# Kernel optimization log

Measured on AMD Instinct MI355X. Metric: run time of the kernel, lower is better.

The kernel has to match this reference:

```python
import jax, jax.numpy as jnp
import numpy as np

N_NODES = 100000
N_EDGES = 1600000
IN_C, HID_C, OUT_C = 128, 128, 64


def gcn_conv(x, W, b, src, dst, n_nodes):
    """PyG-style GCNConv: h = x @ W; add self-loops; symmetric deg^-1/2 norm;
    scatter-add aggregation; + bias. Self-loop contribution added analytically
    (norm for self-loop edge i->i is deg_i^-1) instead of materializing edges."""
    h = x @ W  # [N, C_out]
    # degree over dst including self-loops (edge weights are all ones)
    deg = jax.ops.segment_sum(jnp.ones((src.shape[0],), h.dtype), dst,
                              num_segments=n_nodes) + 1.0
    dinv = jax.lax.rsqrt(deg)  # deg >= 1 always
    norm = dinv[src] * dinv[dst]  # [E]
    agg = jax.ops.segment_sum(h[src] * norm[:, None], dst, num_segments=n_nodes)
    agg = agg + h * (dinv * dinv)[:, None]  # self-loop term
    return agg + b


def setup_inputs() -> dict:
    key = jax.random.key(0)
    k0, k1, k2, k3, k4, k5 = jax.random.split(key, 6)
    x = jax.random.normal(k0, (N_NODES, IN_C), dtype=jnp.float32)
    edge_index = jax.random.randint(k1, (2, N_EDGES), 0, N_NODES, dtype=jnp.int64)
    s1 = 1.0 / np.sqrt(IN_C)
    s2 = 1.0 / np.sqrt(HID_C)
    W1 = jax.random.uniform(k2, (IN_C, HID_C), jnp.float32, -s1, s1)
    b1 = jax.random.uniform(k3, (HID_C,), jnp.float32, -s1, s1)
    W2 = jax.random.uniform(k4, (HID_C, OUT_C), jnp.float32, -s2, s2)
    b2 = jax.random.uniform(k5, (OUT_C,), jnp.float32, -s2, s2)
    return {"x": x, "W1": W1, "b1": b1, "W2": W2, "b2": b2,
            "edge_index": edge_index}


def reference(x, W1, b1, W2, b2, edge_index):
    src, dst = edge_index[0], edge_index[1]
    h = gcn_conv(x, W1, b1, src, dst, N_NODES)
    h = jax.nn.relu(h)
    out = gcn_conv(h, W2, b2, src, dst, N_NODES)
    return out
```

## Files before the change

kernel.cpp:

```cpp
#include <hip/hip_runtime.h>


static constexpr int BSHIFT = 7;
static constexpr int BWIDTH = 1 << BSHIFT;
static constexpr int MAXBUCK = 2048;
static constexpr int NPART = 256;

static constexpr size_t OFF_ROW  = 458752;
static constexpr size_t OFF_CCNT = 925696;
static constexpr size_t OFF_COFF = 937984;
static constexpr size_t OFF_DINV = 962560;
static constexpr size_t OFF_CSR  = 1376256;
static constexpr size_t OFF_HS1  = 8388608;
static constexpr size_t OFF_PART = 35651584;
static constexpr size_t OFF_HS2  = 62914560;
static constexpr size_t OFF_H2   = 75714560;
static constexpr size_t OFF_W1S  = 77811712;
static constexpr size_t OFF_W2S  = 77844480;

__device__ __forceinline__ unsigned short f2bf(float f) {
    unsigned u = __float_as_uint(f);
    u += 0x7fffu + ((u >> 16) & 1u);
    return (unsigned short)(u >> 16);
}

typedef __attribute__((ext_vector_type(8))) short bf16x8;
typedef __attribute__((ext_vector_type(4))) float f32x4;

__device__ __forceinline__ unsigned detect_flag(const unsigned* __restrict__ w) {
    unsigned fl = 0;
#pragma unroll
    for (int k = 1; k < 32; k += 2) fl |= w[k];
    return fl;
}

__device__ __forceinline__ int edge_dst(const unsigned* w, unsigned flag,
                                        int e, int E) {
    return flag ? (int)w[E + e] : (int)w[2 * E + 2 * e];
}
__device__ __forceinline__ int edge_src(const unsigned* w, unsigned flag,
                                        int e, int E) {
    return flag ? (int)w[e] : (int)w[2 * e];
}

__global__ __launch_bounds__(1024) void hist_wprep_kernel(
    const unsigned* __restrict__ w, unsigned* __restrict__ ccnt,
    unsigned* __restrict__ h2, int E, int nbuck,
    const float* __restrict__ W1, const float* __restrict__ W2,
    unsigned short* __restrict__ O1, unsigned short* __restrict__ O2) {
    if (blockIdx.x >= NPART) {
        const int which = blockIdx.x - NPART;
        const float* W = which ? W2 : W1;
        unsigned short* O = which ? O2 : O1;
        const int BN = which ? 64 : 128;
        const int total = 128 * BN / 4;
        for (int g = threadIdx.x; g < total; g += 1024) {
            int n = g % BN, k0 = (g / BN) * 4;
            ushort4 u;
            u.x = f2bf(W[(size_t)(k0 + 0) * BN + n]);
            u.y = f2bf(W[(size_t)(k0 + 1) * BN + n]);
            u.z = f2bf(W[(size_t)(k0 + 2) * BN + n]);
            u.w = f2bf(W[(size_t)(k0 + 3) * BN + n]);
            int off = ((((n >> 4) * 4 + (k0 >> 5)) * 16 + (n & 15)) * 4 +
                       ((k0 >> 3) & 3)) * 8 + (k0 & 4);
            *(ushort4*)(O + off) = u;
        }
        return;
    }
    __shared__ unsigned hist[MAXBUCK];
    for (int i = threadIdx.x; i < nbuck; i += 1024) hist[i] = 0;
    __syncthreads();
    const unsigned f = detect_flag(w);
    const int per = (E + NPART - 1) / NPART;
    const int e0 = blockIdx.x * per, e1 = min(E, e0 + per);
    for (int e = e0 + (int)threadIdx.x; e < e1; e += 1024)
        atomicAdd(&hist[edge_dst(w, f, e, E) >> BSHIFT], 1u);
    __syncthreads();
    for (int i = threadIdx.x; i < nbuck; i += 1024) {
        unsigned h = hist[i];
        h2[(size_t)i * NPART + blockIdx.x] = h;
        if (h) atomicAdd(&ccnt[i], h);
    }
}

__global__ __launch_bounds__(NPART) void scanoff_kernel(
    const unsigned* __restrict__ ccnt, unsigned* __restrict__ coff,
    unsigned* __restrict__ h2, int nbuck) {
    __shared__ unsigned red[NPART];
    __shared__ unsigned sh[NPART];
    const int b = blockIdx.x, t = threadIdx.x;
    unsigned p = 0;
    for (int i = t; i < b; i += NPART) p += ccnt[i];
    red[t] = p;
    __syncthreads();
#pragma unroll
    for (int off = NPART / 2; off > 0; off >>= 1) {
        if (t < off) red[t] += red[t + off];
        __syncthreads();
    }
    const unsigned coffb = red[0];
    if (t == 0) {
        coff[b] = coffb;
        if (b == nbuck - 1) coff[nbuck] = coffb + ccnt[b];
    }
    unsigned v = h2[(size_t)b * NPART + t];
    sh[t] = v;
    __syncthreads();
#pragma unroll
    for (int off = 1; off < NPART; off <<= 1) {
        unsigned a = (t >= off) ? sh[t - off] : 0u;
        __syncthreads();
        sh[t] += a;
        __syncthreads();
    }
    h2[(size_t)b * NPART + t] = coffb + sh[t] - v;
}

__global__ __launch_bounds__(1024) void partition_kernel(
    const unsigned* __restrict__ w, const unsigned* __restrict__ h2,
    unsigned* __restrict__ part, int E, int nbuck) {
    __shared__ unsigned lcur[MAXBUCK];
    for (int i = threadIdx.x; i < nbuck; i += 1024)
        lcur[i] = h2[(size_t)i * NPART + blockIdx.x];
    __syncthreads();
    const unsigned f = detect_flag(w);
    const int per = (E + NPART - 1) / NPART;
    const int e0 = blockIdx.x * per, e1 = min(E, e0 + per);
    for (int e = e0 + (int)threadIdx.x; e < e1; e += 1024) {
        int d = edge_dst(w, f, e, E);
        int s = edge_src(w, f, e, E);
        unsigned pos = atomicAdd(&lcur[d >> BSHIFT], 1u);
        part[pos] = (unsigned)s | ((unsigned)(d & (BWIDTH - 1)) << 20);
    }
}

template <int BN, bool ABF16, bool SCALE>
__device__ __forceinline__ void gemm_body(
    const void* __restrict__ Av, const unsigned short* __restrict__ Bs,
    const float* __restrict__ dinv, unsigned short* __restrict__ out,
    int M, int row0, int t) {
    constexpr int NT = BN / 16;
    const int w = t >> 6, lane = t & 63;
    const int m = lane & 15, q = lane >> 4;
    const int fb = (m * 4 + q) * 8;

    const int r0 = row0 + (2 * w) * 16 + m;
    const int r1 = r0 + 16;

    f32x4 acc[2][NT];
#pragma unroll
    for (int lt = 0; lt < 2; lt++)
#pragma unroll
        for (int nt = 0; nt < NT; nt++) acc[lt][nt] = (f32x4){0.f, 0.f, 0.f, 0.f};

#pragma unroll
    for (int ks = 0; ks < 4; ks++) {
        const int k0 = ks * 32 + q * 8;
        bf16x8 a0 = (bf16x8){0, 0, 0, 0, 0, 0, 0, 0};
        bf16x8 a1 = (bf16x8){0, 0, 0, 0, 0, 0, 0, 0};
        if (ABF16) {
            const unsigned short* A = (const unsigned short*)Av;
            if (r0 < M) a0 = *(const bf16x8*)(A + (size_t)r0 * 128 + k0);
            if (r1 < M) a1 = *(const bf16x8*)(A + (size_t)r1 * 128 + k0);
        } else {
            const float* A = (const float*)Av;
            if (r0 < M) {
                const float* p = A + (size_t)r0 * 128 + k0;
                f32x4 lo = *(const f32x4*)p, hi = *(const f32x4*)(p + 4);
                a0[0] = (short)f2bf(lo[0]); a0[1] = (short)f2bf(lo[1]);
                a0[2] = (short)f2bf(lo[2]); a0[3] = (short)f2bf(lo[3]);
                a0[4] = (short)f2bf(hi[0]); a0[5] = (short)f2bf(hi[1]);
                a0[6] = (short)f2bf(hi[2]); a0[7] = (short)f2bf(hi[3]);
            }
            if (r1 < M) {
                const float* p = A + (size_t)r1 * 128 + k0;
                f32x4 lo = *(const f32x4*)p, hi = *(const f32x4*)(p + 4);
                a1[0] = (short)f2bf(lo[0]); a1[1] = (short)f2bf(lo[1]);
                a1[2] = (short)f2bf(lo[2]); a1[3] = (short)f2bf(lo[3]);
                a1[4] = (short)f2bf(hi[0]); a1[5] = (short)f2bf(hi[1]);
                a1[6] = (short)f2bf(hi[2]); a1[7] = (short)f2bf(hi[3]);
            }
        }
#pragma unroll
        for (int nt = 0; nt < NT; nt++) {
            bf16x8 b = *(const bf16x8*)(Bs + (nt * 4 + ks) * 512 + fb);
            acc[0][nt] = __builtin_amdgcn_mfma_f32_16x16x32_bf16(a0, b, acc[0][nt], 0, 0, 0);
            acc[1][nt] = __builtin_amdgcn_mfma_f32_16x16x32_bf16(a1, b, acc[1][nt], 0, 0, 0);
        }
    }

#pragma unroll
    for (int lt = 0; lt < 2; lt++) {
#pragma unroll
        for (int r = 0; r < 4; r++) {
            int row = row0 + w * 32 + lt * 16 + q * 4 + r;
            if (row < M) {
                float s = SCALE ? dinv[row] : 1.0f;
#pragma unroll
                for (int nt = 0; nt < NT; nt++)
                    out[(size_t)row * BN + nt * 16 + m] = f2bf(acc[lt][nt][r] * s);
            }
        }
    }
}

__global__ __launch_bounds__(256, 4) void bucket_gemm_kernel(
    const unsigned* __restrict__ part, const unsigned* __restrict__ coff,
    unsigned* __restrict__ row, float* __restrict__ dinv,
    int* __restrict__ csr, int N, int nbuck,
    const float* __restrict__ x, const unsigned short* __restrict__ w1s,
    unsigned short* __restrict__ hs1) {
    __shared__ unsigned cnt[BWIDTH];
    __shared__ unsigned sc[BWIDTH];
    __shared__ unsigned cur[BWIDTH];
    const int bid = blockIdx.x, t = threadIdx.x;
    if (bid >= nbuck) {
        gemm_body<128, false, false>(x, w1s, nullptr, hs1, N,
                                     (bid - nbuck) * 128, t);
        return;
    }
    const int b = bid, base = b << BSHIFT;
    if (t < BWIDTH) cnt[t] = 0;
    __syncthreads();
    const int e0 = (int)coff[b], e1 = (int)coff[b + 1];
    for (int e = e0 + t; e < e1; e += 256)
        atomicAdd(&cnt[part[e] >> 20], 1u);
    __syncthreads();
    if (t < BWIDTH) sc[t] = cnt[t];
    __syncthreads();
#pragma unroll
    for (int off = 1; off < BWIDTH; off <<= 1) {
        unsigned a = (t < BWIDTH && t >= off) ? sc[t - off] : 0u;
        __syncthreads();
        if (t < BWIDTH) sc[t] += a;
        __syncthreads();
    }
    if (t < BWIDTH) {
        unsigned r = (unsigned)e0 + sc[t] - cnt[t];
        cur[t] = r;
        if (base + t < N) {
            row[base + t] = r;
            dinv[base + t] = rsqrtf((float)cnt[t] + 1.0f);
        }
    }
    if (t == 0 && b == nbuck - 1) row[N] = (unsigned)e1;
    __syncthreads();
    for (int e = e0 + t; e < e1; e += 256) {
        unsigned pk = part[e];
        unsigned p = atomicAdd(&cur[pk >> 20], 1u);
        csr[p] = (int)(pk & 0xFFFFFu);
    }
}

__global__ __launch_bounds__(256) void agg_gemm_kernel(
    const int* __restrict__ csr, const unsigned* __restrict__ row,
    const unsigned short* __restrict__ hs1, const float* __restrict__ dinv,
    const float* __restrict__ bias, const unsigned short* __restrict__ w2s,
    unsigned short* __restrict__ hs2, int N) {
    __shared__ short sA[2048];
    const int t = threadIdx.x;
    const int i0 = blockIdx.x * 16;
    const int i = i0 + (t >> 4);
    const int l = t & 15;

    float s0 = 0.f, s1 = 0.f, s2 = 0.f, s3 = 0.f,
          s4 = 0.f, s5 = 0.f, s6 = 0.f, s7 = 0.f;
    if (i < N) {
        const int co = 8 * l;
        {
            const float wsf = dinv[i];
            uint4 u = *(const uint4*)(hs1 + (size_t)i * 128 + co);
            s0 += wsf * __uint_as_float(u.x << 16);
            s1 += wsf * __uint_as_float(u.x & 0xffff0000u);
            s2 += wsf * __uint_as_float(u.y << 16);
            s3 += wsf * __uint_as_float(u.y & 0xffff0000u);
            s4 += wsf * __uint_as_float(u.z << 16);
            s5 += wsf * __uint_as_float(u.z & 0xffff0000u);
            s6 += wsf * __uint_as_float(u.w << 16);
            s7 += wsf * __uint_as_float(u.w & 0xffff0000u);
        }
        const int rs = (int)row[i], re = (int)row[i + 1];
        for (int e0 = rs; e0 < re; e0 += 16) {
            int idx = (e0 + l < re) ? csr[e0 + l] : 0;
            const int cnt = min(16, re - e0);
#pragma unroll 4
            for (int j = 0; j < cnt; j++) {
                int s = __shfl(idx, j, 16);
                const float wsr = dinv[s];
                uint4 u = *(const uint4*)(hs1 + (size_t)s * 128 + co);
                s0 += wsr * __uint_as_float(u.x << 16);
                s1 += wsr * __uint_as_float(u.x & 0xffff0000u);
                s2 += wsr * __uint_as_float(u.y << 16);
                s3 += wsr * __uint_as_float(u.y & 0xffff0000u);
                s4 += wsr * __uint_as_float(u.z << 16);
                s5 += wsr * __uint_as_float(u.z & 0xffff0000u);
                s6 += wsr * __uint_as_float(u.w << 16);
                s7 += wsr * __uint_as_float(u.w & 0xffff0000u);
            }
        }
        const float sc = dinv[i];
        const int co2 = 8 * l;
        const float4 ba = *(const float4*)(bias + co2);
        const float4 bb = *(const float4*)(bias + co2 + 4);
        s0 = fmaxf(s0 * sc + ba.x, 0.f); s1 = fmaxf(s1 * sc + ba.y, 0.f);
        s2 = fmaxf(s2 * sc + ba.z, 0.f); s3 = fmaxf(s3 * sc + ba.w, 0.f);
        s4 = fmaxf(s4 * sc + bb.x, 0.f); s5 = fmaxf(s5 * sc + bb.y, 0.f);
        s6 = fmaxf(s6 * sc + bb.z, 0.f); s7 = fmaxf(s7 * sc + bb.w, 0.f);
    } else {
        s0 = s1 = s2 = s3 = s4 = s5 = s6 = s7 = 0.f;
    }
    {
        uint4 u;
        u.x = (unsigned)f2bf(s0) | ((unsigned)f2bf(s1) << 16);
        u.y = (unsigned)f2bf(s2) | ((unsigned)f2bf(s3) << 16);
        u.z = (unsigned)f2bf(s4) | ((unsigned)f2bf(s5) << 16);
        u.w = (unsigned)f2bf(s6) | ((unsigned)f2bf(s7) << 16);
        int off = (l >> 2) * 512 + (((t >> 4) * 4 + (l & 3)) * 8);
        *(uint4*)(sA + off) = u;
    }
    __syncthreads();

    const int w = t >> 6, lane = t & 63;
    const int m = lane & 15, q = lane >> 4;
    const int fb = (m * 4 + q) * 8;
    f32x4 acc = (f32x4){0.f, 0.f, 0.f, 0.f};
#pragma unroll
    for (int ks = 0; ks < 4; ks++) {
        bf16x8 a = *(const bf16x8*)(sA + ks * 512 + fb);
        bf16x8 b = *(const bf16x8*)(w2s + (w * 4 + ks) * 512 + fb);
        acc = __builtin_amdgcn_mfma_f32_16x16x32_bf16(a, b, acc, 0, 0, 0);
    }
#pragma unroll
    for (int r = 0; r < 4; r++) {
        int rr = i0 + q * 4 + r;
        if (rr < N) {
            float s = dinv[rr];
            hs2[(size_t)rr * 64 + w * 16 + m] = f2bf(acc[r] * s);
        }
    }
}

__global__ __launch_bounds__(256) void agg2_kernel(
    const int* __restrict__ csr, const unsigned* __restrict__ row,
    const unsigned short* __restrict__ hsb, const float* __restrict__ dinv,
    const float* __restrict__ bias, float* __restrict__ outv, int N) {
    constexpr int C = 64, LPN = 8;
    const int tid = blockIdx.x * 256 + threadIdx.x;
    const int i = tid / LPN;
    const int l = tid % LPN;
    if (i >= N) return;

    const int co = 8 * l;
    float s0 = 0.f, s1 = 0.f, s2 = 0.f, s3 = 0.f,
          s4 = 0.f, s5 = 0.f, s6 = 0.f, s7 = 0.f;
    {
        uint4 u = *(const uint4*)(hsb + (size_t)i * C + co);
        s0 += __uint_as_float(u.x << 16); s1 += __uint_as_float(u.x & 0xffff0000u);
        s2 += __uint_as_float(u.y << 16); s3 += __uint_as_float(u.y & 0xffff0000u);
        s4 += __uint_as_float(u.z << 16); s5 += __uint_as_float(u.z & 0xffff0000u);
        s6 += __uint_as_float(u.w << 16); s7 += __uint_as_float(u.w & 0xffff0000u);
    }

    const int rs = (int)row[i], re = (int)row[i + 1];
    for (int e0 = rs; e0 < re; e0 += LPN) {
        int idx = (e0 + l < re) ? csr[e0 + l] : 0;
        const int cnt = min(LPN, re - e0);
#pragma unroll 4
        for (int j = 0; j < cnt; j++) {
            int s = __shfl(idx, j, LPN);
            uint4 u = *(const uint4*)(hsb + (size_t)s * C + co);
            s0 += __uint_as_float(u.x << 16); s1 += __uint_as_float(u.x & 0xffff0000u);
            s2 += __uint_as_float(u.y << 16); s3 += __uint_as_float(u.y & 0xffff0000u);
            s4 += __uint_as_float(u.z << 16); s5 += __uint_as_float(u.z & 0xffff0000u);
            s6 += __uint_as_float(u.w << 16); s7 += __uint_as_float(u.w & 0xffff0000u);
        }
    }

    const float sc = dinv[i];
    const float4 ba = *(const float4*)(bias + co);
    const float4 bb = *(const float4*)(bias + co + 4);
    float4 a = make_float4(s0 * sc + ba.x, s1 * sc + ba.y,
                           s2 * sc + ba.z, s3 * sc + ba.w);
    float4 b = make_float4(s4 * sc + bb.x, s5 * sc + bb.y,
                           s6 * sc + bb.z, s7 * sc + bb.w);
    *(float4*)(outv + (size_t)i * C + co) = a;
    *(float4*)(outv + (size_t)i * C + co + 4) = b;
}

extern "C" void kernel_launch(void* const* d_in, const int* in_sizes, int n_in,
                              void* d_out, int out_size, void* d_ws,
                              size_t ws_size, hipStream_t stream) {
    const float* x  = (const float*)d_in[0];
    const float* W1 = (const float*)d_in[1];
    const float* b1 = (const float*)d_in[2];
    const float* W2 = (const float*)d_in[3];
    const float* b2 = (const float*)d_in[4];
    const unsigned* ew = (const unsigned*)d_in[5];
    const int E = in_sizes[5] / 2;
    const int N = in_sizes[0] / 128;
    const int nbuck = (N + BWIDTH - 1) >> BSHIFT;

    char* ws = (char*)d_ws;
    unsigned* row  = (unsigned*)(ws + OFF_ROW);
    unsigned* ccnt = (unsigned*)(ws + OFF_CCNT);
    unsigned* coff = (unsigned*)(ws + OFF_COFF);
    float* dinv    = (float*)(ws + OFF_DINV);
    int* csr       = (int*)(ws + OFF_CSR);
    unsigned short* hs1  = (unsigned short*)(ws + OFF_HS1);
    unsigned short* hs2  = (unsigned short*)(ws + OFF_HS2);
    unsigned* h2   = (unsigned*)(ws + OFF_H2);
    unsigned short* w1s  = (unsigned short*)(ws + OFF_W1S);
    unsigned short* w2s  = (unsigned short*)(ws + OFF_W2S);
    unsigned* part = (unsigned*)(ws + OFF_PART);

    hipMemsetAsync(ccnt, 0, (size_t)(nbuck + 1) * 4, stream);

    hist_wprep_kernel<<<NPART + 2, 1024, 0, stream>>>(ew, ccnt, h2, E, nbuck,
                                                      W1, W2, w1s, w2s);
    scanoff_kernel<<<nbuck, NPART, 0, stream>>>(ccnt, coff, h2, nbuck);
    partition_kernel<<<NPART, 1024, 0, stream>>>(ew, h2, part, E, nbuck);
    bucket_gemm_kernel<<<nbuck + (N + 127) / 128, 256, 0, stream>>>(
        part, coff, row, dinv, csr, N, nbuck, x, w1s, hs1);

    agg_gemm_kernel<<<(N + 15) / 16, 256, 0, stream>>>(
        csr, row, hs1, dinv, b1, w2s, hs2, N);

    agg2_kernel<<<(N * 8 + 255) / 256, 256, 0, stream>>>(
        csr, row, hs2, dinv, b2, (float*)d_out, N);
}
```

Baseline: 267.9 us.

## Fold bucket offset scan into partition kernel, drop memset and scan launch

Removes the memset, the global atomic bucket totals and the separate scan kernel. Each partition block now recomputes the per-bucket prefix over partitions and the total counts from the histogram matrix, then scans the totals in shared memory before partitioning. This saves two launches and global atomics. In exchange, every one of the 256 blocks redundantly reads the whole nbuck x 256 histogram (~800KB each) and runs a 1024-wide shared scan, which lengthens the partition kernel's prologue.

```diff
diff --git a/kernel.cpp b/kernel.cpp
--- a/kernel.cpp
+++ b/kernel.cpp
@@ -7,7 +7,6 @@
 static constexpr int NPART = 256;
 
 static constexpr size_t OFF_ROW  = 458752;
-static constexpr size_t OFF_CCNT = 925696;
 static constexpr size_t OFF_COFF = 937984;
 static constexpr size_t OFF_DINV = 962560;
 static constexpr size_t OFF_CSR  = 1376256;
@@ -44,9 +43,8 @@
 }
 
 __global__ __launch_bounds__(1024) void hist_wprep_kernel(
-    const unsigned* __restrict__ w, unsigned* __restrict__ ccnt,
-    unsigned* __restrict__ h2, int E, int nbuck,
-    const float* __restrict__ W1, const float* __restrict__ W2,
+    const unsigned* __restrict__ w, unsigned* __restrict__ h2, int E,
+    int nbuck, const float* __restrict__ W1, const float* __restrict__ W2,
     unsigned short* __restrict__ O1, unsigned short* __restrict__ O2) {
     if (blockIdx.x >= NPART) {
         const int which = blockIdx.x - NPART;
@@ -76,57 +74,55 @@
     for (int e = e0 + (int)threadIdx.x; e < e1; e += 1024)
         atomicAdd(&hist[edge_dst(w, f, e, E) >> BSHIFT], 1u);
     __syncthreads();
-    for (int i = threadIdx.x; i < nbuck; i += 1024) {
-        unsigned h = hist[i];
-        h2[(size_t)i * NPART + blockIdx.x] = h;
-        if (h) atomicAdd(&ccnt[i], h);
-    }
-}
-
-__global__ __launch_bounds__(NPART) void scanoff_kernel(
-    const unsigned* __restrict__ ccnt, unsigned* __restrict__ coff,
-    unsigned* __restrict__ h2, int nbuck) {
-    __shared__ unsigned red[NPART];
-    __shared__ unsigned sh[NPART];
-    const int b = blockIdx.x, t = threadIdx.x;
-    unsigned p = 0;
-    for (int i = t; i < b; i += NPART) p += ccnt[i];
-    red[t] = p;
-    __syncthreads();
-#pragma unroll
-    for (int off = NPART / 2; off > 0; off >>= 1) {
-        if (t < off) red[t] += red[t + off];
-        __syncthreads();
-    }
-    const unsigned coffb = red[0];
-    if (t == 0) {
-        coff[b] = coffb;
-        if (b == nbuck - 1) coff[nbuck] = coffb + ccnt[b];
-    }
-    unsigned v = h2[(size_t)b * NPART + t];
-    sh[t] = v;
-    __syncthreads();
-#pragma unroll
-    for (int off = 1; off < NPART; off <<= 1) {
-        unsigned a = (t >= off) ? sh[t - off] : 0u;
-        __syncthreads();
-        sh[t] += a;
-        __syncthreads();
-    }
-    h2[(size_t)b * NPART + t] = coffb + sh[t] - v;
+    for (int i = threadIdx.x; i < nbuck; i += 1024)
+        h2[(size_t)i * NPART + blockIdx.x] = hist[i];
 }
 
 __global__ __launch_bounds__(1024) void partition_kernel(
     const unsigned* __restrict__ w, const unsigned* __restrict__ h2,
-    unsigned* __restrict__ part, int E, int nbuck) {
+    unsigned* __restrict__ coff, unsigned* __restrict__ part, int E,
+    int nbuck) {
     __shared__ unsigned lcur[MAXBUCK];
-    for (int i = threadIdx.x; i < nbuck; i += 1024)
-        lcur[i] = h2[(size_t)i * NPART + blockIdx.x];
+    __shared__ unsigned tot[MAXBUCK];
+    __shared__ unsigned sh[1024];
+    const int blk = blockIdx.x, t = threadIdx.x;
+    for (int i = t; i < nbuck; i += 1024) {
+        const unsigned* hrow = h2 + (size_t)i * NPART;
+        unsigned cs = 0, tt = 0;
+        for (int c = 0; c < NPART; c++) {
+            unsigned v = hrow[c];
+            cs += (c < blk) ? v : 0u;
+            tt += v;
+        }
+        lcur[i] = cs;
+        tot[i] = tt;
+    }
+    __syncthreads();
+    unsigned run = 0;
+    for (int b0 = 0; b0 < nbuck; b0 += 1024) {
+        unsigned v = (b0 + t < nbuck) ? tot[b0 + t] : 0u;
+        sh[t] = v;
+        __syncthreads();
+        for (int off = 1; off < 1024; off <<= 1) {
+            unsigned a = (t >= off) ? sh[t - off] : 0u;
+            __syncthreads();
+            sh[t] += a;
+            __syncthreads();
+        }
+        if (b0 + t < nbuck) {
+            unsigned coffb = run + sh[t] - v;
+            lcur[b0 + t] += coffb;
+            if (blk == 0) coff[b0 + t] = coffb;
+        }
+        run += sh[1023];
+        __syncthreads();
+    }
+    if (blk == 0 && t == 0) coff[nbuck] = run;
     __syncthreads();
     const unsigned f = detect_flag(w);
     const int per = (E + NPART - 1) / NPART;
-    const int e0 = blockIdx.x * per, e1 = min(E, e0 + per);
-    for (int e = e0 + (int)threadIdx.x; e < e1; e += 1024) {
+    const int e0 = blk * per, e1 = min(E, e0 + per);
+    for (int e = e0 + t; e < e1; e += 1024) {
         int d = edge_dst(w, f, e, E);
         int s = edge_src(w, f, e, E);
         unsigned pos = atomicAdd(&lcur[d >> BSHIFT], 1u);
@@ -402,7 +398,6 @@
 
     char* ws = (char*)d_ws;
     unsigned* row  = (unsigned*)(ws + OFF_ROW);
-    unsigned* ccnt = (unsigned*)(ws + OFF_CCNT);
     unsigned* coff = (unsigned*)(ws + OFF_COFF);
     float* dinv    = (float*)(ws + OFF_DINV);
     int* csr       = (int*)(ws + OFF_CSR);
@@ -413,12 +408,9 @@
     unsigned short* w2s  = (unsigned short*)(ws + OFF_W2S);
     unsigned* part = (unsigned*)(ws + OFF_PART);
 
-    hipMemsetAsync(ccnt, 0, (size_t)(nbuck + 1) * 4, stream);
-
-    hist_wprep_kernel<<<NPART + 2, 1024, 0, stream>>>(ew, ccnt, h2, E, nbuck,
+    hist_wprep_kernel<<<NPART + 2, 1024, 0, stream>>>(ew, h2, E, nbuck,
                                                       W1, W2, w1s, w2s);
-    scanoff_kernel<<<nbuck, NPART, 0, stream>>>(ccnt, coff, h2, nbuck);
-    partition_kernel<<<NPART, 1024, 0, stream>>>(ew, h2, part, E, nbuck);
+    partition_kernel<<<NPART, 1024, 0, stream>>>(ew, h2, coff, part, E, nbuck);
     bucket_gemm_kernel<<<nbuck + (N + 127) / 128, 256, 0, stream>>>(
         part, coff, row, dinv, csr, N, nbuck, x, w1s, hs1);
 
```

New measurement: 281.1 us. +4.9%, slower.
